# Kernel optimization log

Measured on AMD Instinct MI355X. Metric: run time of the kernel, lower is better.

## Reference

```python
import jax, jax.numpy as jnp
import numpy as np
from jax import lax

TEMPERATURE = 34.0
PAD = 1

def setup_inputs() -> dict:
    key = jax.random.key(0)
    ks = jax.random.split(key, 6)
    B, C, H, W = 16, 256, 64, 64
    K, O, kk, hidden = 4, 256, 3, int(256 * 0.25) + 1
    return {
        "x": jax.random.normal(ks[0], (B, C, H, W), jnp.float32),
        "w_fc1": jax.random.normal(ks[1], (hidden, C), jnp.float32) * 0.05,
        "w_fc2": jax.random.normal(ks[2], (K, hidden), jnp.float32) * 0.05,
        "b_fc2": jax.random.normal(ks[3], (K,), jnp.float32) * 0.05,
        "weight": jax.random.normal(ks[4], (K, O, C, kk, kk), jnp.float32) * 0.05,
        "bias": jax.random.normal(ks[5], (K, O), jnp.float32) * 0.05,
    }

def reference(x, w_fc1, w_fc2, b_fc2, weight, bias):
    # attention2d: global avg pool -> 1x1 conv -> relu -> 1x1 conv -> softmax(logits/T)
    pooled = jnp.mean(x, axis=(2, 3))                       # [B, C]
    h = jax.nn.relu(pooled @ w_fc1.T)                       # [B, hidden]
    logits = h @ w_fc2.T + b_fc2                            # [B, K]
    att = jax.nn.softmax(logits / TEMPERATURE, axis=1)      # [B, K]

    K = weight.shape[0]
    # per-sample aggregated kernels/bias
    agg_w = jnp.einsum('bk,koihw->boihw', att, weight)      # [B, O, C, k, k]
    agg_b = att @ bias                                      # [B, O]

    def conv_one(xi, wi):
        # xi: [C, H, W], wi: [O, C, k, k]
        return lax.conv_general_dilated(
            xi[None], wi, window_strides=(1, 1),
            padding=[(PAD, PAD), (PAD, PAD)],
            dimension_numbers=('NCHW', 'OIHW', 'NCHW'))[0]

    out = jax.vmap(conv_one)(x, agg_w)                      # [B, O, H, W]
    return out + agg_b[:, :, None, None]
```

## Files before the change

kernel.cpp:

```cpp
#include <hip/hip_runtime.h>
#include <math.h>

constexpr int B   = 16;
constexpr int C   = 256;
constexpr int H   = 64;
constexpr int W   = 64;
constexpr int K   = 4;
constexpr int O   = 256;
constexpr int HID = 65;
constexpr float TEMP = 34.0f;

typedef __bf16 bf16x8 __attribute__((ext_vector_type(8)));
typedef float  f32x16 __attribute__((ext_vector_type(16)));
typedef unsigned short ushort_t;

__device__ inline ushort_t f2bf(float f) {
    union { float f; unsigned u; } v; v.f = f;
    unsigned u = v.u;
    u += 0x7FFF + ((u >> 16) & 1);
    return (ushort_t)(u >> 16);
}

__device__ inline void gl2lds16(const void* g, void* l) {
    __builtin_amdgcn_global_load_lds(
        (const __attribute__((address_space(1))) unsigned int*)g,
        (__attribute__((address_space(3))) unsigned int*)l, 16, 0, 0);
}

__global__ void tp_kernel(const float* __restrict__ x,
                          ushort_t* __restrict__ xT,
                          float* __restrict__ pooled) {
    const int ci = blockIdx.x, yg = blockIdx.y, b = blockIdx.z;
    const int tid = threadIdx.x;
    const int lane = tid & 63;

    __shared__ ushort_t t2[8 * 1154];
    __shared__ float pool_l[16];
    if (tid < 16) pool_l[tid] = 0.f;
    __syncthreads();

    const float* xbase = x + ((size_t)b * C + ci * 16) * (H * W);

    #pragma unroll
    for (int j = 0; j < 8; ++j) {
        const int idx = j * 256 + tid;
        const int xq = idx & 15;
        const int y8 = (idx >> 4) & 7;
        const int c  = idx >> 7;
        float4 v = *(const float4*)(xbase + ((size_t)c * H + (yg * 8 + y8)) * W + xq * 4);
        float s = (v.x + v.y) + (v.z + v.w);
        s += __shfl_xor(s, 1, 64);
        s += __shfl_xor(s, 2, 64);
        s += __shfl_xor(s, 4, 64);
        s += __shfl_xor(s, 8, 64);
        if ((lane & 15) == 0) atomicAdd(&pool_l[c], s);
        ushort_t* d = &t2[y8 * 1154 + (xq * 4) * 18 + c];
        d[0]  = f2bf(v.x);
        d[18] = f2bf(v.y);
        d[36] = f2bf(v.z);
        d[54] = f2bf(v.w);
    }
    __syncthreads();

    #pragma unroll
    for (int q = 0; q < 4; ++q) {
        const int e = q * 256 + tid;
        const int y8 = e >> 7, col = (e >> 1) & 63, half = e & 1;
        const ushort_t* s0 = &t2[y8 * 1154 + col * 18 + half * 8];
        uint4 vv;
        vv.x = *(const unsigned*)(s0 + 0);
        vv.y = *(const unsigned*)(s0 + 2);
        vv.z = *(const unsigned*)(s0 + 4);
        vv.w = *(const unsigned*)(s0 + 6);
        size_t go = (((size_t)(b * 16 + ci) * 64) + (yg * 8 + y8)) * 1024
                  + col * 16 + half * 8;
        *(uint4*)(xT + go) = vv;
    }
    if (tid < 16)
        atomicAdd(&pooled[b * C + ci * 16 + tid], pool_l[tid] * (1.0f / (H * W)));
}

__global__ void attention_kernel(const float* __restrict__ pooled,
                                 const float* __restrict__ w_fc1,
                                 const float* __restrict__ w_fc2,
                                 const float* __restrict__ b_fc2,
                                 float* __restrict__ att) {
    const int b = blockIdx.x;
    const int tid = threadIdx.x;
    __shared__ float pool_s[C];
    __shared__ float h_s[HID];
    __shared__ float logit_s[K];

    for (int i = tid; i < C; i += blockDim.x) pool_s[i] = pooled[b * C + i];
    __syncthreads();
    for (int j = tid; j < HID; j += blockDim.x) {
        const float* wr = w_fc1 + (size_t)j * C;
        float s = 0.f;
        #pragma unroll 4
        for (int c = 0; c < C; ++c) s += pool_s[c] * wr[c];
        h_s[j] = fmaxf(s, 0.f);
    }
    __syncthreads();
    if (tid < K) {
        const float* wr = w_fc2 + (size_t)tid * HID;
        float s = b_fc2[tid];
        for (int j = 0; j < HID; ++j) s += h_s[j] * wr[j];
        logit_s[tid] = s * (1.0f / TEMP);
    }
    __syncthreads();
    if (tid == 0) {
        float m = fmaxf(fmaxf(logit_s[0], logit_s[1]), fmaxf(logit_s[2], logit_s[3]));
        float e0 = expf(logit_s[0] - m), e1 = expf(logit_s[1] - m);
        float e2 = expf(logit_s[2] - m), e3 = expf(logit_s[3] - m);
        float inv = 1.0f / (e0 + e1 + e2 + e3);
        att[b * K + 0] = e0 * inv; att[b * K + 1] = e1 * inv;
        att[b * K + 2] = e2 * inv; att[b * K + 3] = e3 * inv;
    }
}

__global__ void wagg_kernel(const float* __restrict__ weight,
                            const float* __restrict__ att,
                            ushort_t* __restrict__ wagg_sw) {
    const int ci = blockIdx.x;
    const int mi = blockIdx.y;
    const int tid = threadIdx.x;
    const int lane = tid & 63;
    const int wid  = tid >> 6;

    __shared__ float lds_w[4 * 32 * 145];
    __shared__ float att_s[B * K];

    if (tid < B * K) att_s[tid] = att[tid];

    for (int idx = tid; idx < 128 * 36; idx += 256) {
        const int seg = idx / 36;
        const int off = idx - seg * 36;
        const int k = seg >> 5, o = seg & 31;
        const float4 v = *(const float4*)(weight
            + ((size_t)(k * O + mi * 32 + o) * C + ci * 16) * 9 + off * 4);
        float* d = &lds_w[seg * 145 + off * 4];
        d[0] = v.x; d[1] = v.y; d[2] = v.z; d[3] = v.w;
    }
    __syncthreads();

    const int o_l = lane & 31;
    const int cc0 = (lane >> 5) * 8;
    for (int task = wid; task < B * 9; task += 4) {
        const int b = task / 9, t = task - b * 9;
        const float a0 = att_s[b * K + 0], a1 = att_s[b * K + 1];
        const float a2 = att_s[b * K + 2], a3 = att_s[b * K + 3];
        union { ushort_t u[8]; uint4 v; } pk;
        #pragma unroll
        for (int j = 0; j < 8; ++j) {
            const int m = (cc0 + j) * 9 + t;
            pk.u[j] = f2bf(a0 * lds_w[(0 * 32 + o_l) * 145 + m]
                         + a1 * lds_w[(1 * 32 + o_l) * 145 + m]
                         + a2 * lds_w[(2 * 32 + o_l) * 145 + m]
                         + a3 * lds_w[(3 * 32 + o_l) * 145 + m]);
        }
        size_t idx = ((((size_t)b * 16 + ci) * 9 + t) * 8 + mi) * 512 + lane * 8;
        *(uint4*)&wagg_sw[idx] = pk.v;
    }
}

__global__ __launch_bounds__(256, 2)
void conv_mfma_kernel(const ushort_t* __restrict__ xT,
                      const ushort_t* __restrict__ wagg_sw,
                      const float* __restrict__ bias,
                      const float* __restrict__ att,
                      float* __restrict__ out) {
    const int b  = blockIdx.x;
    const int yt = blockIdx.y;
    const int oz = blockIdx.z;
    const int y0 = yt * 4;

    const int tid  = threadIdx.x;
    const int lane = tid & 63;
    const int wid  = tid >> 6;
    const int n16  = lane & 31;
    const int khalf = lane >> 5;

    __shared__ __align__(16) ushort_t A_lds[9 * 4 * 512];
    __shared__ __align__(16) ushort_t x_lds[6 * 1056];

    for (int i = tid; i < 6 * 1056; i += 256) x_lds[i] = 0;

    f32x16 acc[4][2];
    #pragma unroll
    for (int a = 0; a < 4; ++a)
        #pragma unroll
        for (int ni = 0; ni < 2; ++ni)
            acc[a][ni] = (f32x16)(0.f);

    for (int ci = 0; ci < 16; ++ci) {
        __syncthreads();

        for (int i = wid; i < 36; i += 4) {
            const int t = i >> 2, a = i & 3;
            const ushort_t* g = wagg_sw
                + ((((size_t)b * 16 + ci) * 9 + t) * 8 + (oz * 4 + a)) * 512 + lane * 8;
            gl2lds16(g, &A_lds[(t * 4 + a) * 512]);
        }
        for (int r = wid; r < 6; r += 4) {
            const int y = y0 - 1 + r;
            if ((unsigned)y < (unsigned)H) {
                const ushort_t* gr = xT + (((size_t)(b * 16 + ci) * 64 + y) * 1024);
                #pragma unroll
                for (int h = 0; h < 2; ++h)
                    gl2lds16(gr + lane * 16 + h * 8,
                             &x_lds[r * 1056 + h * 528 + 8]);
            }
        }

        __syncthreads();

        #pragma unroll
        for (int dy = 0; dy < 3; ++dy) {
            const int r = wid + dy;
            #pragma unroll
            for (int dx = 0; dx < 3; ++dx) {
                const int t = dy * 3 + dx;
                bf16x8 bf[2];
                #pragma unroll
                for (int ni = 0; ni < 2; ++ni)
                    bf[ni] = *(const bf16x8*)&x_lds[r * 1056 + khalf * 528
                              + (ni * 32 + n16 + dx) * 8];
                #pragma unroll
                for (int a = 0; a < 4; ++a) {
                    bf16x8 af = *(const bf16x8*)&A_lds[(t * 4 + a) * 512 + lane * 8];
                    acc[a][0] = __builtin_amdgcn_mfma_f32_32x32x16_bf16(af, bf[0], acc[a][0], 0, 0, 0);
                    acc[a][1] = __builtin_amdgcn_mfma_f32_32x32x16_bf16(af, bf[1], acc[a][1], 0, 0, 0);
                }
            }
        }
    }

    __syncthreads();
    float* aggb = (float*)A_lds;
    if (tid < 128) {
        const int o = oz * 128 + tid;
        aggb[tid] = att[b * K + 0] * bias[0 * O + o] + att[b * K + 1] * bias[1 * O + o]
                  + att[b * K + 2] * bias[2 * O + o] + att[b * K + 3] * bias[3 * O + o];
    }
    __syncthreads();

    const int y = y0 + wid;
    #pragma unroll
    for (int a = 0; a < 4; ++a) {
        #pragma unroll
        for (int ni = 0; ni < 2; ++ni) {
            #pragma unroll
            for (int reg = 0; reg < 16; ++reg) {
                const int row = (reg & 3) + 8 * (reg >> 2) + 4 * khalf;
                const int ol  = a * 32 + row;
                out[(((size_t)b * O + oz * 128 + ol) * H + y) * W + ni * 32 + n16]
                    = acc[a][ni][reg] + aggb[ol];
            }
        }
    }
}

__global__ void pool_kernel(const float* __restrict__ x, float* __restrict__ pooled) {
    const int bc = blockIdx.x;
    const float4* p4 = (const float4*)(x + (size_t)bc * (H * W));
    const int tid = threadIdx.x;
    float s = 0.f;
    #pragma unroll
    for (int i = 0; i < (H * W / 4) / 256; ++i) {
        float4 v = p4[tid + i * 256];
        s += (v.x + v.y) + (v.z + v.w);
    }
    #pragma unroll
    for (int off = 32; off > 0; off >>= 1) s += __shfl_down(s, off, 64);
    __shared__ float red[4];
    if ((tid & 63) == 0) red[tid >> 6] = s;
    __syncthreads();
    if (tid == 0) pooled[bc] = ((red[0] + red[1]) + (red[2] + red[3])) * (1.0f / (H * W));
}

constexpr int TILE_H = 32;
constexpr int TILE_W = 64;
constexpr int CCF = 4, OT = 8, PX = 8;
constexpr int XS_STRIDE = TILE_W + 3;

__global__ __launch_bounds__(256, 2)
void conv_kernel(const float* __restrict__ x, const float* __restrict__ weight,
                 const float* __restrict__ bias, const float* __restrict__ att,
                 float* __restrict__ out) {
    const int tile_y = blockIdx.x, o0 = blockIdx.y * OT, b = blockIdx.z;
    const int tid = threadIdx.x, tx = tid & 7, ty = tid >> 3, ty0 = tile_y * TILE_H;
    __shared__ __align__(16) float xs[CCF][TILE_H + 2][XS_STRIDE];
    __shared__ __align__(16) float ws_s[OT][CCF][12];
    const float a0 = att[b * K + 0], a1 = att[b * K + 1];
    const float a2 = att[b * K + 2], a3 = att[b * K + 3];
    float acc[OT][PX];
    #pragma unroll
    for (int o = 0; o < OT; ++o)
        #pragma unroll
        for (int p = 0; p < PX; ++p) acc[o][p] = 0.f;
    const float* xb = x + (size_t)b * C * H * W;
    constexpr int X_ELEMS = CCF * (TILE_H + 2) * (TILE_W + 2);
    constexpr int W_ELEMS = OT * CCF * 9;
    for (int c0 = 0; c0 < C; c0 += CCF) {
        __syncthreads();
        for (int idx = tid; idx < X_ELEMS; idx += 256) {
            int cc = idx / ((TILE_H + 2) * (TILE_W + 2));
            int rem = idx - cc * ((TILE_H + 2) * (TILE_W + 2));
            int r = rem / (TILE_W + 2), col = rem - r * (TILE_W + 2);
            int gy = ty0 - 1 + r, gx = col - 1;
            float v = 0.f;
            if ((unsigned)gy < (unsigned)H && (unsigned)gx < (unsigned)W)
                v = xb[((size_t)(c0 + cc) * H + gy) * W + gx];
            xs[cc][r][col] = v;
        }
        for (int idx = tid; idx < W_ELEMS; idx += 256) {
            int o = idx / (CCF * 9), rem = idx - o * (CCF * 9);
            int cc = rem / 9, tap = rem - cc * 9;
            size_t base = ((size_t)(o0 + o) * C + (c0 + cc)) * 9 + tap;
            ws_s[o][cc][tap] = a0 * weight[base] + a1 * weight[(size_t)1 * O * C * 9 + base]
                             + a2 * weight[(size_t)2 * O * C * 9 + base]
                             + a3 * weight[(size_t)3 * O * C * 9 + base];
        }
        __syncthreads();
        #pragma unroll
        for (int cc = 0; cc < CCF; ++cc) {
            float xv[3][10];
            #pragma unroll
            for (int dy = 0; dy < 3; ++dy)
                #pragma unroll
                for (int j = 0; j < 10; ++j) xv[dy][j] = xs[cc][ty + dy][8 * tx + j];
            #pragma unroll
            for (int o = 0; o < OT; ++o) {
                float4 w0 = *(const float4*)&ws_s[o][cc][0];
                float4 w1 = *(const float4*)&ws_s[o][cc][4];
                float w8 = ws_s[o][cc][8];
                #pragma unroll
                for (int p = 0; p < PX; ++p) {
                    float s = acc[o][p];
                    s = fmaf(xv[0][p + 0], w0.x, s); s = fmaf(xv[0][p + 1], w0.y, s);
                    s = fmaf(xv[0][p + 2], w0.z, s); s = fmaf(xv[1][p + 0], w0.w, s);
                    s = fmaf(xv[1][p + 1], w1.x, s); s = fmaf(xv[1][p + 2], w1.y, s);
                    s = fmaf(xv[2][p + 0], w1.z, s); s = fmaf(xv[2][p + 1], w1.w, s);
                    s = fmaf(xv[2][p + 2], w8, s);
                    acc[o][p] = s;
                }
            }
        }
    }
    const int oy = ty0 + ty, ox = 8 * tx;
    #pragma unroll
    for (int o = 0; o < OT; ++o) {
        float ab = a0 * bias[0 * O + o0 + o] + a1 * bias[1 * O + o0 + o]
                 + a2 * bias[2 * O + o0 + o] + a3 * bias[3 * O + o0 + o];
        float4 v0 = make_float4(acc[o][0] + ab, acc[o][1] + ab, acc[o][2] + ab, acc[o][3] + ab);
        float4 v1 = make_float4(acc[o][4] + ab, acc[o][5] + ab, acc[o][6] + ab, acc[o][7] + ab);
        float* op = out + (((size_t)b * O + (o0 + o)) * H + oy) * W + ox;
        *(float4*)(op) = v0; *(float4*)(op + 4) = v1;
    }
}

extern "C" void kernel_launch(void* const* d_in, const int* in_sizes, int n_in,
                              void* d_out, int out_size, void* d_ws, size_t ws_size,
                              hipStream_t stream) {
    const float* x      = (const float*)d_in[0];
    const float* w_fc1  = (const float*)d_in[1];
    const float* w_fc2  = (const float*)d_in[2];
    const float* b_fc2  = (const float*)d_in[3];
    const float* weight = (const float*)d_in[4];
    const float* bias   = (const float*)d_in[5];
    float* out = (float*)d_out;

    float* pooled = (float*)d_ws;
    float* att    = pooled + B * C;
    ushort_t* wagg_sw = (ushort_t*)((char*)d_ws + 32 * 1024);
    const size_t wagg_bytes = (size_t)B * 16 * 9 * 8 * 512 * 2;
    ushort_t* xT = (ushort_t*)((char*)wagg_sw + wagg_bytes);
    const size_t xT_bytes = (size_t)B * 16 * 64 * 64 * 16 * 2;
    const size_t needed = 32 * 1024 + wagg_bytes + xT_bytes;

    if (ws_size >= needed) {
        hipMemsetAsync(pooled, 0, B * C * sizeof(float), stream);
        tp_kernel<<<dim3(16, 8, 16), dim3(256), 0, stream>>>(x, xT, pooled);
        attention_kernel<<<dim3(B), dim3(128), 0, stream>>>(pooled, w_fc1, w_fc2, b_fc2, att);
        wagg_kernel<<<dim3(16, 8), dim3(256), 0, stream>>>(weight, att, wagg_sw);
        conv_mfma_kernel<<<dim3(B, 16, 2), dim3(256), 0, stream>>>(xT, wagg_sw, bias, att, out);
    } else {
        pool_kernel<<<dim3(B * C), dim3(256), 0, stream>>>(x, pooled);
        attention_kernel<<<dim3(B), dim3(128), 0, stream>>>(pooled, w_fc1, w_fc2, b_fc2, att);
        conv_kernel<<<dim3(H / TILE_H, O / OT, B), dim3(256), 0, stream>>>(x, weight, bias, att, out);
    }
}
```

Baseline: 219.7 us.

## Fuse attention into weight aggregation and double-buffer conv weight staging

Removes the separate attention kernel launch: every wagg block now recomputes the pooled MLP and softmax redundantly, and block (0,0) writes att for later use. The conv kernel double-buffers the aggregated-weight LDS tiles, prefetching the next channel group during the current MFMA loop with explicit vmcnt waits. It also drops LDS staging of x and reads the input rows straight from global memory, with clamped indices and explicit zeroing at the borders. This trades one launch and LDS traffic for redundant MLP work in 128 blocks, uncoalesced per-lane global reads of x, and a read of att in the conv epilogue that depends on block (0,0) of the previous kernel.

```diff
diff --git a/kernel.cpp b/kernel.cpp
--- a/kernel.cpp
+++ b/kernel.cpp
@@ -19,6 +19,12 @@
     unsigned u = v.u;
     u += 0x7FFF + ((u >> 16) & 1);
     return (ushort_t)(u >> 16);
+}
+
+__device__ inline bf16x8 bf8_zero() {
+    union { uint4 u; bf16x8 v; } z;
+    z.u = make_uint4(0u, 0u, 0u, 0u);
+    return z.v;
 }
 
 __device__ inline void gl2lds16(const void* g, void* l) {
@@ -119,7 +125,11 @@
 }
 
 __global__ void wagg_kernel(const float* __restrict__ weight,
-                            const float* __restrict__ att,
+                            const float* __restrict__ pooled,
+                            const float* __restrict__ w_fc1,
+                            const float* __restrict__ w_fc2,
+                            const float* __restrict__ b_fc2,
+                            float* __restrict__ att,
                             ushort_t* __restrict__ wagg_sw) {
     const int ci = blockIdx.x;
     const int mi = blockIdx.y;
@@ -128,9 +138,43 @@
     const int wid  = tid >> 6;
 
     __shared__ float lds_w[4 * 32 * 145];
+    __shared__ float pool_a[B * C];
+    __shared__ float h_s[B * HID];
+    __shared__ float logit_s[B * K];
     __shared__ float att_s[B * K];
 
-    if (tid < B * K) att_s[tid] = att[tid];
+    for (int i = tid; i < B * C; i += 256) pool_a[i] = pooled[i];
+    __syncthreads();
+    for (int task = tid; task < B * HID; task += 256) {
+        const int bb = task / HID, j = task - bb * HID;
+        const float* wr = w_fc1 + (size_t)j * C;
+        const float* pr = pool_a + bb * C;
+        float s = 0.f;
+        #pragma unroll 4
+        for (int c = 0; c < C; ++c) s += pr[c] * wr[c];
+        h_s[bb * HID + j] = fmaxf(s, 0.f);
+    }
+    __syncthreads();
+    if (tid < B * K) {
+        const int bb = tid >> 2, k = tid & 3;
+        const float* wr = w_fc2 + (size_t)k * HID;
+        float s = b_fc2[k];
+        for (int j = 0; j < HID; ++j) s += h_s[bb * HID + j] * wr[j];
+        logit_s[tid] = s * (1.0f / TEMP);
+    }
+    __syncthreads();
+    if (tid < B) {
+        const float l0 = logit_s[tid * 4 + 0], l1 = logit_s[tid * 4 + 1];
+        const float l2 = logit_s[tid * 4 + 2], l3 = logit_s[tid * 4 + 3];
+        const float m = fmaxf(fmaxf(l0, l1), fmaxf(l2, l3));
+        const float e0 = expf(l0 - m), e1 = expf(l1 - m);
+        const float e2 = expf(l2 - m), e3 = expf(l3 - m);
+        const float inv = 1.0f / (e0 + e1 + e2 + e3);
+        att_s[tid * 4 + 0] = e0 * inv; att_s[tid * 4 + 1] = e1 * inv;
+        att_s[tid * 4 + 2] = e2 * inv; att_s[tid * 4 + 3] = e3 * inv;
+    }
+    __syncthreads();
+    if (ci == 0 && mi == 0 && tid < B * K) att[tid] = att_s[tid];
 
     for (int idx = tid; idx < 128 * 36; idx += 256) {
         const int seg = idx / 36;
@@ -180,10 +224,8 @@
     const int n16  = lane & 31;
     const int khalf = lane >> 5;
 
-    __shared__ __align__(16) ushort_t A_lds[9 * 4 * 512];
-    __shared__ __align__(16) ushort_t x_lds[6 * 1056];
-
-    for (int i = tid; i < 6 * 1056; i += 256) x_lds[i] = 0;
+    __shared__ __align__(16) ushort_t A_lds[2][36 * 512];
+    __shared__ float aggb[128];
 
     f32x16 acc[4][2];
     #pragma unroll
@@ -192,51 +234,62 @@
         for (int ni = 0; ni < 2; ++ni)
             acc[a][ni] = (f32x16)(0.f);
 
-    for (int ci = 0; ci < 16; ++ci) {
-        __syncthreads();
-
+    auto stageA = [&](int ci, int buf) {
         for (int i = wid; i < 36; i += 4) {
             const int t = i >> 2, a = i & 3;
             const ushort_t* g = wagg_sw
                 + ((((size_t)b * 16 + ci) * 9 + t) * 8 + (oz * 4 + a)) * 512 + lane * 8;
-            gl2lds16(g, &A_lds[(t * 4 + a) * 512]);
-        }
-        for (int r = wid; r < 6; r += 4) {
-            const int y = y0 - 1 + r;
+            gl2lds16(g, &A_lds[buf][i * 512]);
+        }
+    };
+
+    stageA(0, 0);
+
+    for (int ci = 0; ci < 16; ++ci) {
+        const int cur = ci & 1;
+        if (ci < 15) {
+            stageA(ci + 1, cur ^ 1);
+            asm volatile("s_waitcnt vmcnt(9)" ::: "memory");
+        } else {
+            asm volatile("s_waitcnt vmcnt(0)" ::: "memory");
+        }
+        __builtin_amdgcn_s_barrier();
+
+        const ushort_t* xci = xT + ((size_t)(b * 16 + ci) * 64) * 1024;
+        #pragma unroll
+        for (int dy = 0; dy < 3; ++dy) {
+            const int y = y0 + wid + dy - 1;
             if ((unsigned)y < (unsigned)H) {
-                const ushort_t* gr = xT + (((size_t)(b * 16 + ci) * 64 + y) * 1024);
+                const ushort_t* xrow = xci + (size_t)y * 1024;
+                bf16x8 bf[3][2];
                 #pragma unroll
-                for (int h = 0; h < 2; ++h)
-                    gl2lds16(gr + lane * 16 + h * 8,
-                             &x_lds[r * 1056 + h * 528 + 8]);
-            }
-        }
-
-        __syncthreads();
-
-        #pragma unroll
-        for (int dy = 0; dy < 3; ++dy) {
-            const int r = wid + dy;
-            #pragma unroll
-            for (int dx = 0; dx < 3; ++dx) {
-                const int t = dy * 3 + dx;
-                bf16x8 bf[2];
+                for (int dx = 0; dx < 3; ++dx) {
+                    #pragma unroll
+                    for (int ni = 0; ni < 2; ++ni) {
+                        const int col  = ni * 32 + n16 + dx - 1;
+                        const int colc = col < 0 ? 0 : (col > 63 ? 63 : col);
+                        bf16x8 v = *(const bf16x8*)&xrow[colc * 16 + khalf * 8];
+                        if ((dx == 0 && ni == 0 && n16 == 0) ||
+                            (dx == 2 && ni == 1 && n16 == 31))
+                            v = bf8_zero();
+                        bf[dx][ni] = v;
+                    }
+                }
                 #pragma unroll
-                for (int ni = 0; ni < 2; ++ni)
-                    bf[ni] = *(const bf16x8*)&x_lds[r * 1056 + khalf * 528
-                              + (ni * 32 + n16 + dx) * 8];
-                #pragma unroll
-                for (int a = 0; a < 4; ++a) {
-                    bf16x8 af = *(const bf16x8*)&A_lds[(t * 4 + a) * 512 + lane * 8];
-                    acc[a][0] = __builtin_amdgcn_mfma_f32_32x32x16_bf16(af, bf[0], acc[a][0], 0, 0, 0);
-                    acc[a][1] = __builtin_amdgcn_mfma_f32_32x32x16_bf16(af, bf[1], acc[a][1], 0, 0, 0);
+                for (int dx = 0; dx < 3; ++dx) {
+                    const int t = dy * 3 + dx;
+                    #pragma unroll
+                    for (int a = 0; a < 4; ++a) {
+                        bf16x8 af = *(const bf16x8*)&A_lds[cur][(t * 4 + a) * 512 + lane * 8];
+                        acc[a][0] = __builtin_amdgcn_mfma_f32_32x32x16_bf16(af, bf[dx][0], acc[a][0], 0, 0, 0);
+                        acc[a][1] = __builtin_amdgcn_mfma_f32_32x32x16_bf16(af, bf[dx][1], acc[a][1], 0, 0, 0);
+                    }
                 }
             }
         }
-    }
-
-    __syncthreads();
-    float* aggb = (float*)A_lds;
+        __builtin_amdgcn_s_barrier();
+    }
+
     if (tid < 128) {
         const int o = oz * 128 + tid;
         aggb[tid] = att[b * K + 0] * bias[0 * O + o] + att[b * K + 1] * bias[1 * O + o]
@@ -381,8 +434,7 @@
     if (ws_size >= needed) {
         hipMemsetAsync(pooled, 0, B * C * sizeof(float), stream);
         tp_kernel<<<dim3(16, 8, 16), dim3(256), 0, stream>>>(x, xT, pooled);
-        attention_kernel<<<dim3(B), dim3(128), 0, stream>>>(pooled, w_fc1, w_fc2, b_fc2, att);
-        wagg_kernel<<<dim3(16, 8), dim3(256), 0, stream>>>(weight, att, wagg_sw);
+        wagg_kernel<<<dim3(16, 8), dim3(256), 0, stream>>>(weight, pooled, w_fc1, w_fc2, b_fc2, att, wagg_sw);
         conv_mfma_kernel<<<dim3(B, 16, 2), dim3(256), 0, stream>>>(xT, wagg_sw, bias, att, out);
     } else {
         pool_kernel<<<dim3(B * C), dim3(256), 0, stream>>>(x, pooled);
```

Measured after the change: 256.6 us. 16.8% more time.
